# Optimization experiments

Hardware: AMD Instinct MI355X
Metric: run time of the kernel (lower is better)

The kernel has to match this reference:

```python
import jax, jax.numpy as jnp
import numpy as np

N_FEATURES = 1024
N_HEADS = 16
DEPTH = N_FEATURES // N_HEADS


def setup_inputs() -> dict:
    key = jax.random.key(0)
    ks = jax.random.split(key, 12)
    B, S, D = 2, 2048, N_FEATURES
    s = 1.0 / np.sqrt(D)
    return {
        "q": jax.random.normal(ks[0], (B, S, D), jnp.float32),
        "k": jax.random.normal(ks[1], (B, S, D), jnp.float32),
        "v": jax.random.normal(ks[2], (B, S, D), jnp.float32),
        "w_q": jax.random.normal(ks[3], (D, D), jnp.float32) * s,
        "b_q": jnp.zeros((D,), jnp.float32),
        "w_k": jax.random.normal(ks[4], (D, D), jnp.float32) * s,
        "b_k": jnp.zeros((D,), jnp.float32),
        "w_v": jax.random.normal(ks[5], (D, D), jnp.float32) * s,
        "b_v": jnp.zeros((D,), jnp.float32),
        "w_o": jax.random.normal(ks[6], (D, D), jnp.float32) * s,
        "b_o": jnp.zeros((D,), jnp.float32),
    }


def _split_heads(x):
    # [B, S, D] -> [B, H, S, depth]
    B, S, _ = x.shape
    return x.reshape(B, S, N_HEADS, DEPTH).transpose(0, 2, 1, 3)


def reference(q, k, v, w_q, b_q, w_k, b_k, w_v, b_v, w_o, b_o):
    B, S, D = q.shape
    qh = _split_heads(q @ w_q + b_q)  # [B,H,S,d]
    kh = _split_heads(k @ w_k + b_k)
    vh = _split_heads(v @ w_v + b_v)
    scale = 1.0 / jnp.sqrt(jnp.asarray(DEPTH, jnp.float32))
    logits = jnp.einsum("bhqd,bhkd->bhqk", qh, kh) * scale  # [B,H,S,S]
    attn_weights = jax.nn.softmax(logits, axis=-1)
    attn = jnp.einsum("bhqk,bhkd->bhqd", attn_weights, vh)
    concat = attn.transpose(0, 2, 1, 3).reshape(B, S, D)
    output = concat @ w_o + b_o
    return output, attn_weights
```

## Files before the change

kernel.cpp:

```cpp
#include <hip/hip_runtime.h>

typedef __attribute__((ext_vector_type(8))) short short8;
typedef __attribute__((ext_vector_type(4))) float f32x4;

#define MFMA_BF16(A,B,C) __builtin_amdgcn_mfma_f32_16x16x32_bf16((A),(B),(C),0,0,0)

#define SCALE_LOG2E 0.18033688011112043f

__device__ __forceinline__ unsigned short f2bu(float f) {
  unsigned int u = __float_as_uint(f);
  u += 0x7fffu + ((u >> 16) & 1u);
  return (unsigned short)(u >> 16);
}
__device__ __forceinline__ float bu2f(unsigned short u) {
  return __uint_as_float(((unsigned int)u) << 16);
}
__device__ __forceinline__ void gload16(const void* g, void* l) {
  __builtin_amdgcn_global_load_lds(
      (const __attribute__((address_space(1))) void*)g,
      (__attribute__((address_space(3))) void*)l, 16, 0, 0);
}
#define WAITV0 asm volatile("s_waitcnt vmcnt(0)" ::: "memory")
#define WAITV4 asm volatile("s_waitcnt vmcnt(4)" ::: "memory")
__device__ __forceinline__ void barrier_fence() {
  __builtin_amdgcn_s_barrier();
  __builtin_amdgcn_sched_barrier(0);
}

struct PrepArgs {
  const float* src[7];
  unsigned short* dst[7];
};
__global__ __launch_bounds__(256) void prep_kernel(PrepArgs a) {
  __shared__ float t[32][33];
  if (blockIdx.y < 3) {
    const int w = blockIdx.y;
    const int i = blockIdx.x * 256 + threadIdx.x;
    const float4 v = reinterpret_cast<const float4*>(a.src[w])[i];
    ushort4 o;
    o.x = f2bu(v.x); o.y = f2bu(v.y); o.z = f2bu(v.z); o.w = f2bu(v.w);
    reinterpret_cast<ushort4*>(a.dst[w])[i] = o;
  } else {
    const int m = blockIdx.x >> 10;
    const float* w = a.src[3 + m];
    unsigned short* wt = a.dst[3 + m];
    const int bx = ((blockIdx.x >> 5) & 31) * 32;
    const int by = (blockIdx.x & 31) * 32;
    const int tx = threadIdx.x & 31, ty = threadIdx.x >> 5;
    for (int j = 0; j < 4; ++j)
      t[ty + 8 * j][tx] = w[(size_t)(bx + ty + 8 * j) * 1024 + by + tx];
    __syncthreads();
    for (int j = 0; j < 4; ++j)
      wt[(size_t)(by + ty + 8 * j) * 1024 + bx + tx] = f2bu(t[tx][ty + 8 * j]);
  }
}

template <int OUT_MODE>
__device__ __forceinline__ void gemm_core(
    unsigned short* g_lds,
    const unsigned short* __restrict__ A, const unsigned short* __restrict__ Wt,
    const float* __restrict__ bias, void* __restrict__ Cout, int M0, int N0) {
  const int tid = threadIdx.x, lane = tid & 63, wid = tid >> 6;
  const int lr = lane & 15, lg = lane >> 4;
  const int wr = wid >> 2, wc = wid & 3;
  const int srow = lane >> 3, slot = lane & 7;
  f32x4 acc[4][2];
#pragma unroll
  for (int m = 0; m < 4; ++m)
#pragma unroll
    for (int n = 0; n < 2; ++n) acc[m][n] = (f32x4){0.f, 0.f, 0.f, 0.f};

#define G_STAGE(buf, kk)                                                             \
  {                                                                                  \
    _Pragma("unroll") for (int i_ = 0; i_ < 2; ++i_) {                               \
      int idx_ = wid * 2 + i_;                                                       \
      int row_ = idx_ * 8 + srow;                                                    \
      int gs_ = slot ^ (row_ & 7);                                                   \
      gload16(&A[(size_t)(M0 + row_) * 1024 + (kk) + gs_ * 8],                       \
              (char*)g_lds + (buf) * 32768 + idx_ * 1024);                           \
      gload16(&Wt[(size_t)(N0 + row_) * 1024 + (kk) + gs_ * 8],                      \
              (char*)g_lds + (buf) * 32768 + 16384 + idx_ * 1024);                   \
    }                                                                                \
  }

  G_STAGE(0, 0);
  __syncthreads();
  for (int kt = 0; kt < 16; ++kt) {
    const int cur = kt & 1;
    if (kt < 15) G_STAGE(cur ^ 1, (kt + 1) * 64);
    short8 af[4][2], bf[2][2];
#pragma unroll
    for (int m = 0; m < 4; ++m)
#pragma unroll
      for (int kh = 0; kh < 2; ++kh) {
        int row = wr * 64 + m * 16 + lr;
        int s = (kh * 4 + lg) ^ (row & 7);
        af[m][kh] = *reinterpret_cast<const short8*>((const char*)g_lds + cur * 32768 + row * 128 + s * 16);
      }
#pragma unroll
    for (int n = 0; n < 2; ++n)
#pragma unroll
      for (int kh = 0; kh < 2; ++kh) {
        int row = wc * 32 + n * 16 + lr;
        int s = (kh * 4 + lg) ^ (row & 7);
        bf[n][kh] = *reinterpret_cast<const short8*>((const char*)g_lds + cur * 32768 + 16384 + row * 128 + s * 16);
      }
#pragma unroll
    for (int kh = 0; kh < 2; ++kh)
#pragma unroll
      for (int m = 0; m < 4; ++m)
#pragma unroll
        for (int n = 0; n < 2; ++n)
          acc[m][n] = MFMA_BF16(af[m][kh], bf[n][kh], acc[m][n]);
    __syncthreads();
  }

  if (OUT_MODE != 2) {
#pragma unroll
    for (int m = 0; m < 4; ++m)
#pragma unroll
      for (int n = 0; n < 2; ++n)
#pragma unroll
        for (int r = 0; r < 4; ++r) {
          int grow = M0 + wr * 64 + m * 16 + lg * 4 + r;
          int gcol = N0 + wc * 32 + n * 16 + lr;
          float vv = acc[m][n][r] + bias[gcol];
          if (OUT_MODE == 1)
            reinterpret_cast<float*>(Cout)[(size_t)grow * 1024 + gcol] = vv;
          else
            reinterpret_cast<unsigned short*>(Cout)[(size_t)grow * 1024 + gcol] = f2bu(vv);
        }
  } else {
    unsigned short* t = g_lds;
#pragma unroll
    for (int m = 0; m < 4; ++m)
#pragma unroll
      for (int n = 0; n < 2; ++n) {
        int ch = wc * 32 + n * 16 + lr;
        int s4 = wr * 64 + m * 16 + lg * 4;
        int sb = (s4 * 2) ^ ((ch & 7) << 4);
        ushort4 pk;
        pk.x = f2bu(acc[m][n][0] + bias[N0 + ch]);
        pk.y = f2bu(acc[m][n][1] + bias[N0 + ch]);
        pk.z = f2bu(acc[m][n][2] + bias[N0 + ch]);
        pk.w = f2bu(acc[m][n][3] + bias[N0 + ch]);
        *reinterpret_cast<ushort4*>((char*)t + ch * 256 + sb) = pk;
      }
    __syncthreads();
    unsigned short* Vt = (unsigned short*)Cout;
    const int ch = tid >> 2, sc = tid & 3;
    const int bb = M0 >> 11;
    unsigned short* dst = Vt + (size_t)(bb * 1024 + N0 + ch) * 2048 + (M0 & 2047) + sc * 8;
#pragma unroll
    for (int i = 0; i < 4; ++i) {
      int sb = (sc * 16 + i * 64) ^ ((ch & 7) << 4);
      short8 v = *reinterpret_cast<const short8*>((const char*)t + ch * 256 + sb);
      *reinterpret_cast<short8*>(dst + i * 32) = v;
    }
  }
#undef G_STAGE
}

struct Gemm3Args {
  const unsigned short* A[3]; const unsigned short* Wt[3];
  const float* bias[3]; void* C[3];
};
__global__ __launch_bounds__(512) void gemm3_kernel(Gemm3Args a) {
  __shared__ unsigned short g_lds[2 * 16384];
  const int z = blockIdx.z;
  if (z == 2)
    gemm_core<2>(g_lds, a.A[2], a.Wt[2], a.bias[2], a.C[2], blockIdx.x * 128, blockIdx.y * 128);
  else
    gemm_core<0>(g_lds, a.A[z], a.Wt[z], a.bias[z], a.C[z], blockIdx.x * 128, blockIdx.y * 128);
}

__global__ __launch_bounds__(512) void gemm_out_kernel(
    const unsigned short* __restrict__ A, const unsigned short* __restrict__ Wt,
    const float* __restrict__ bias, float* __restrict__ C) {
  __shared__ unsigned short g_lds[2 * 16384];
  gemm_core<1>(g_lds, A, Wt, bias, C, blockIdx.x * 128, blockIdx.y * 128);
}

__global__ __launch_bounds__(512) void attn_den_kernel(
    const unsigned short* __restrict__ Qp, const unsigned short* __restrict__ Kp,
    float* __restrict__ invl_g) {
  __shared__ unsigned short k_lds[2][8192];
  const int bid = ((blockIdx.x & 7) << 6) | (blockIdx.x >> 3);
  const int qt = bid & 15, h = (bid >> 4) & 15, b = bid >> 8;
  const int tid = threadIdx.x, lane = tid & 63, wid = tid >> 6;
  const int lr = lane & 15, lg = lane >> 4;
  const int q0 = qt * 128;
  const int srow = lane >> 3, slot = lane & 7;

  short8 aq[2];
#pragma unroll
  for (int kh = 0; kh < 2; ++kh)
    aq[kh] = *reinterpret_cast<const short8*>(
        &Qp[(size_t)(b * 2048 + q0 + wid * 16 + lr) * 1024 + h * 64 + kh * 32 + lg * 8]);

  const size_t kbase = (size_t)b * 2048 * 1024 + (size_t)(h * 64);

#define KD_STAGE(buf, kk)                                                         \
  {                                                                               \
    _Pragma("unroll") for (int i_ = 0; i_ < 2; ++i_) {                            \
      int idx_ = wid * 2 + i_;                                                    \
      int row_ = idx_ * 8 + srow;                                                 \
      int gs_ = slot ^ (row_ & 7);                                                \
      gload16(&Kp[kbase + (size_t)((kk) + row_) * 1024 + gs_ * 8],                \
              (char*)&k_lds[buf][0] + idx_ * 1024);                               \
    }                                                                             \
  }

  float lsum[4] = {0.f, 0.f, 0.f, 0.f};

  KD_STAGE(0, 0);
  WAITV0;
  barrier_fence();
  for (int kt = 0; kt < 16; ++kt) {
    const int cur = kt & 1;
    if (kt < 15) KD_STAGE(cur ^ 1, (kt + 1) * 128);
    f32x4 lacc[8];
#pragma unroll
    for (int nt = 0; nt < 8; ++nt) lacc[nt] = (f32x4){0.f, 0.f, 0.f, 0.f};
#pragma unroll
    for (int kh = 0; kh < 2; ++kh)
#pragma unroll
      for (int nt = 0; nt < 8; ++nt) {
        int row = nt * 16 + lr;
        int s = (kh * 4 + lg) ^ (row & 7);
        short8 kb = *reinterpret_cast<const short8*>((const char*)&k_lds[cur][0] + row * 128 + s * 16);
        lacc[nt] = MFMA_BF16(aq[kh], kb, lacc[nt]);
      }
#pragma unroll
    for (int nt = 0; nt < 8; ++nt)
#pragma unroll
      for (int r = 0; r < 4; ++r)
        lsum[r] += exp2f(lacc[nt][r] * SCALE_LOG2E);
    WAITV0;
    barrier_fence();
  }
#pragma unroll
  for (int r = 0; r < 4; ++r) {
    float s = lsum[r];
    s += __shfl_xor(s, 1); s += __shfl_xor(s, 2);
    s += __shfl_xor(s, 4); s += __shfl_xor(s, 8);
    if (lr == 0) invl_g[bid * 128 + wid * 16 + lg * 4 + r] = 1.f / s;
  }
#undef KD_STAGE
}

__global__ __launch_bounds__(512) void attn_pv_kernel(
    const unsigned short* __restrict__ Qp, const unsigned short* __restrict__ Kp,
    const unsigned short* __restrict__ Vt, const float* __restrict__ invl_g,
    float* __restrict__ attnw, unsigned short* __restrict__ attnc) {
  __shared__ unsigned short k_lds[2][4096];
  __shared__ unsigned short vt_lds[2][4096];
  __shared__ unsigned short w_lds[8][16][68];
  const int bid = ((blockIdx.x & 7) << 6) | (blockIdx.x >> 3);
  const int qt = bid & 15, h = (bid >> 4) & 15, b = bid >> 8;
  const int tid = threadIdx.x, lane = tid & 63, wid = tid >> 6;
  const int lr = lane & 15, lg = lane >> 4;
  const int q0 = qt * 128;
  const int srow = lane >> 3, slot = lane & 7;

  short8 aq[2];
#pragma unroll
  for (int kh = 0; kh < 2; ++kh)
    aq[kh] = *reinterpret_cast<const short8*>(
        &Qp[(size_t)(b * 2048 + q0 + wid * 16 + lr) * 1024 + h * 64 + kh * 32 + lg * 8]);

  const f32x4 invl = *reinterpret_cast<const f32x4*>(&invl_g[bid * 128 + wid * 16 + lg * 4]);
  float inv_j[4];
#pragma unroll
  for (int j = 0; j < 4; ++j) inv_j[j] = invl_g[bid * 128 + wid * 16 + 4 * j + lg];

  const size_t kbase = (size_t)b * 2048 * 1024 + (size_t)(h * 64);
  const size_t vtbase = (size_t)(b * 1024 + h * 64) * 2048;

#define K_STAGE(buf, kk)                                                          \
  {                                                                               \
    int row_ = wid * 8 + srow;                                                    \
    int gs_ = slot ^ (row_ & 7);                                                  \
    gload16(&Kp[kbase + (size_t)((kk) + row_) * 1024 + gs_ * 8],                  \
            (char*)&k_lds[buf][0] + wid * 1024);                                  \
  }
#define V_STAGE(buf, kk)                                                          \
  {                                                                               \
    int row_ = wid * 8 + srow;                                                    \
    int gs_ = slot ^ (row_ & 7);                                                  \
    gload16(&Vt[vtbase + (size_t)row_ * 2048 + (kk) + gs_ * 8],                   \
            (char*)&vt_lds[buf][0] + wid * 1024);                                 \
  }

  f32x4 oacc[4];
#pragma unroll
  for (int nt = 0; nt < 4; ++nt) oacc[nt] = (f32x4){0.f, 0.f, 0.f, 0.f};

  const size_t wrowb = (size_t)((b * 16 + h) * 2048) + q0 + wid * 16;

  K_STAGE(0, 0);
  V_STAGE(0, 0);
  WAITV0;
  barrier_fence();
  for (int kt = 0; kt < 32; ++kt) {
    const int cur = kt & 1;
    const int k0 = kt * 64;
    if (kt < 31) { K_STAGE(cur ^ 1, k0 + 64); V_STAGE(cur ^ 1, k0 + 64); }
    f32x4 lacc[4];
#pragma unroll
    for (int nt = 0; nt < 4; ++nt) lacc[nt] = (f32x4){0.f, 0.f, 0.f, 0.f};
#pragma unroll
    for (int kh = 0; kh < 2; ++kh)
#pragma unroll
      for (int nt = 0; nt < 4; ++nt) {
        int row = nt * 16 + lr;
        int s = (kh * 4 + lg) ^ (row & 7);
        short8 kb = *reinterpret_cast<const short8*>((const char*)&k_lds[cur][0] + row * 128 + s * 16);
        lacc[nt] = MFMA_BF16(aq[kh], kb, lacc[nt]);
      }
#pragma unroll
    for (int nt = 0; nt < 4; ++nt)
#pragma unroll
      for (int r = 0; r < 4; ++r)
        w_lds[wid][lg * 4 + r][nt * 16 + lr] = f2bu(exp2f(lacc[nt][r] * SCALE_LOG2E));
#pragma unroll
    for (int ks = 0; ks < 2; ++ks) {
      short8 wa = *reinterpret_cast<const short8*>(&w_lds[wid][lr][ks * 32 + lg * 8]);
#pragma unroll
      for (int nt = 0; nt < 4; ++nt) {
        int row = nt * 16 + lr;
        int s = (ks * 4 + lg) ^ (row & 7);
        short8 vb = *reinterpret_cast<const short8*>((const char*)&vt_lds[cur][0] + row * 128 + s * 16);
        oacc[nt] = MFMA_BF16(wa, vb, oacc[nt]);
      }
    }
#pragma unroll
    for (int j = 0; j < 4; ++j) {
      int rowl = 4 * j + lg;
      ushort4 wv = *reinterpret_cast<const ushort4*>(&w_lds[wid][rowl][lr * 4]);
      f32x4 o;
      o[0] = bu2f(wv.x) * inv_j[j];
      o[1] = bu2f(wv.y) * inv_j[j];
      o[2] = bu2f(wv.z) * inv_j[j];
      o[3] = bu2f(wv.w) * inv_j[j];
      __builtin_nontemporal_store(o, reinterpret_cast<f32x4*>(&attnw[(wrowb + rowl) * 2048 + k0 + lr * 4]));
    }
    WAITV4;
    barrier_fence();
  }
#pragma unroll
  for (int nt = 0; nt < 4; ++nt)
#pragma unroll
    for (int r = 0; r < 4; ++r) {
      int srow2 = q0 + wid * 16 + lg * 4 + r;
      attnc[(size_t)(b * 2048 + srow2) * 1024 + h * 64 + nt * 16 + lr] =
          f2bu(oacc[nt][r] * invl[r]);
    }
#undef K_STAGE
#undef V_STAGE
}

extern "C" void kernel_launch(void* const* d_in, const int* in_sizes, int n_in,
                              void* d_out, int out_size, void* d_ws, size_t ws_size,
                              hipStream_t stream) {
  const float* q = (const float*)d_in[0];
  const float* k = (const float*)d_in[1];
  const float* v = (const float*)d_in[2];
  const float* w_q = (const float*)d_in[3];
  const float* b_q = (const float*)d_in[4];
  const float* w_k = (const float*)d_in[5];
  const float* b_k = (const float*)d_in[6];
  const float* w_v = (const float*)d_in[7];
  const float* b_v = (const float*)d_in[8];
  const float* w_o = (const float*)d_in[9];
  const float* b_o = (const float*)d_in[10];

  unsigned short* ws = (unsigned short*)d_ws;
  unsigned short* Qp    = ws;
  unsigned short* Kp    = ws + 4194304;
  unsigned short* Vt    = ws + 8388608;
  unsigned short* attnc = ws + 12582912;
  unsigned short* wqt = ws + 16777216;
  unsigned short* wkt = wqt + 1048576;
  unsigned short* wvt = wkt + 1048576;
  unsigned short* wot = wvt + 1048576;
  float* invl_g = (float*)wqt;

  float* outO = (float*)d_out;
  float* attnw = outO + 4194304;

  unsigned short* qb = (unsigned short*)attnw;
  unsigned short* kb = qb + 4194304;
  unsigned short* vb = kb + 4194304;

  PrepArgs pa;
  pa.src[0] = q; pa.src[1] = k; pa.src[2] = v;
  pa.src[3] = w_q; pa.src[4] = w_k; pa.src[5] = w_v; pa.src[6] = w_o;
  pa.dst[0] = qb; pa.dst[1] = kb; pa.dst[2] = vb;
  pa.dst[3] = wqt; pa.dst[4] = wkt; pa.dst[5] = wvt; pa.dst[6] = wot;
  prep_kernel<<<dim3(4096, 4), 256, 0, stream>>>(pa);

  Gemm3Args ga;
  ga.A[0] = qb; ga.A[1] = kb; ga.A[2] = vb;
  ga.Wt[0] = wqt; ga.Wt[1] = wkt; ga.Wt[2] = wvt;
  ga.bias[0] = b_q; ga.bias[1] = b_k; ga.bias[2] = b_v;
  ga.C[0] = Qp; ga.C[1] = Kp; ga.C[2] = Vt;
  gemm3_kernel<<<dim3(32, 8, 3), 512, 0, stream>>>(ga);

  attn_den_kernel<<<512, 512, 0, stream>>>(Qp, Kp, invl_g);
  attn_pv_kernel<<<512, 512, 0, stream>>>(Qp, Kp, Vt, invl_g, attnw, attnc);

  gemm_out_kernel<<<dim3(32, 8), 512, 0, stream>>>(attnc, wot, b_o, outO);
}
```

Baseline: 229.3 us.

## Fuse attention denominator and PV passes into one kernel with shared LDS

Merges the separate softmax-denominator kernel and the weights/PV kernel into one kernel. The first phase computes row sums of exp(logits), reduces them and keeps the reciprocal in LDS instead of a global buffer, and the second phase reuses the same LDS region for K/V staging. MFMA operands are swapped so each lane holds a whole row segment, which gives a simpler cross-lane reduction and allows packed bf16 conversion (v_cvt_pk_bf16_f32) with vectorised LDS writes of the weights. This removes a kernel launch and a global round trip for the denominators, but each block now runs both passes back to back and uses more LDS.

```diff
diff --git a/kernel.cpp b/kernel.cpp
--- a/kernel.cpp
+++ b/kernel.cpp
@@ -14,6 +14,11 @@
 }
 __device__ __forceinline__ float bu2f(unsigned short u) {
   return __uint_as_float(((unsigned int)u) << 16);
+}
+__device__ __forceinline__ unsigned int cvtpk(float a, float b) {
+  unsigned int r;
+  asm("v_cvt_pk_bf16_f32 %0, %1, %2" : "=v"(r) : "v"(a), "v"(b));
+  return r;
 }
 __device__ __forceinline__ void gload16(const void* g, void* l) {
   __builtin_amdgcn_global_load_lds(
@@ -181,16 +186,20 @@
   gemm_core<1>(g_lds, A, Wt, bias, C, blockIdx.x * 128, blockIdx.y * 128);
 }
 
-__global__ __launch_bounds__(512) void attn_den_kernel(
+__global__ __launch_bounds__(512) void attn_kernel(
     const unsigned short* __restrict__ Qp, const unsigned short* __restrict__ Kp,
-    float* __restrict__ invl_g) {
-  __shared__ unsigned short k_lds[2][8192];
+    const unsigned short* __restrict__ Vt, float* __restrict__ attnw,
+    unsigned short* __restrict__ attnc) {
+  __shared__ unsigned short kv_lds[32768 / 2];
+  __shared__ unsigned short w_lds[8][16][72];
+  __shared__ float linv_lds[128];
   const int bid = ((blockIdx.x & 7) << 6) | (blockIdx.x >> 3);
   const int qt = bid & 15, h = (bid >> 4) & 15, b = bid >> 8;
   const int tid = threadIdx.x, lane = tid & 63, wid = tid >> 6;
   const int lr = lane & 15, lg = lane >> 4;
   const int q0 = qt * 128;
   const int srow = lane >> 3, slot = lane & 7;
+  char* kv = (char*)kv_lds;
 
   short8 aq[2];
 #pragma unroll
@@ -199,6 +208,7 @@
         &Qp[(size_t)(b * 2048 + q0 + wid * 16 + lr) * 1024 + h * 64 + kh * 32 + lg * 8]);
 
   const size_t kbase = (size_t)b * 2048 * 1024 + (size_t)(h * 64);
+  const size_t vtbase = (size_t)(b * 1024 + h * 64) * 2048;
 
 #define KD_STAGE(buf, kk)                                                         \
   {                                                                               \
@@ -207,12 +217,11 @@
       int row_ = idx_ * 8 + srow;                                                 \
       int gs_ = slot ^ (row_ & 7);                                                \
       gload16(&Kp[kbase + (size_t)((kk) + row_) * 1024 + gs_ * 8],                \
-              (char*)&k_lds[buf][0] + idx_ * 1024);                               \
+              kv + (buf) * 16384 + idx_ * 1024);                                  \
     }                                                                             \
   }
 
-  float lsum[4] = {0.f, 0.f, 0.f, 0.f};
-
+  float lsum = 0.f;
   KD_STAGE(0, 0);
   WAITV0;
   barrier_fence();
@@ -228,68 +237,41 @@
       for (int nt = 0; nt < 8; ++nt) {
         int row = nt * 16 + lr;
         int s = (kh * 4 + lg) ^ (row & 7);
-        short8 kb = *reinterpret_cast<const short8*>((const char*)&k_lds[cur][0] + row * 128 + s * 16);
-        lacc[nt] = MFMA_BF16(aq[kh], kb, lacc[nt]);
+        short8 kb = *reinterpret_cast<const short8*>(kv + cur * 16384 + row * 128 + s * 16);
+        lacc[nt] = MFMA_BF16(kb, aq[kh], lacc[nt]);
       }
 #pragma unroll
     for (int nt = 0; nt < 8; ++nt)
 #pragma unroll
       for (int r = 0; r < 4; ++r)
-        lsum[r] += exp2f(lacc[nt][r] * SCALE_LOG2E);
+        lsum += exp2f(lacc[nt][r] * SCALE_LOG2E);
     WAITV0;
     barrier_fence();
   }
-#pragma unroll
-  for (int r = 0; r < 4; ++r) {
-    float s = lsum[r];
-    s += __shfl_xor(s, 1); s += __shfl_xor(s, 2);
-    s += __shfl_xor(s, 4); s += __shfl_xor(s, 8);
-    if (lr == 0) invl_g[bid * 128 + wid * 16 + lg * 4 + r] = 1.f / s;
-  }
-#undef KD_STAGE
-}
-
-__global__ __launch_bounds__(512) void attn_pv_kernel(
-    const unsigned short* __restrict__ Qp, const unsigned short* __restrict__ Kp,
-    const unsigned short* __restrict__ Vt, const float* __restrict__ invl_g,
-    float* __restrict__ attnw, unsigned short* __restrict__ attnc) {
-  __shared__ unsigned short k_lds[2][4096];
-  __shared__ unsigned short vt_lds[2][4096];
-  __shared__ unsigned short w_lds[8][16][68];
-  const int bid = ((blockIdx.x & 7) << 6) | (blockIdx.x >> 3);
-  const int qt = bid & 15, h = (bid >> 4) & 15, b = bid >> 8;
-  const int tid = threadIdx.x, lane = tid & 63, wid = tid >> 6;
-  const int lr = lane & 15, lg = lane >> 4;
-  const int q0 = qt * 128;
-  const int srow = lane >> 3, slot = lane & 7;
-
-  short8 aq[2];
-#pragma unroll
-  for (int kh = 0; kh < 2; ++kh)
-    aq[kh] = *reinterpret_cast<const short8*>(
-        &Qp[(size_t)(b * 2048 + q0 + wid * 16 + lr) * 1024 + h * 64 + kh * 32 + lg * 8]);
-
-  const f32x4 invl = *reinterpret_cast<const f32x4*>(&invl_g[bid * 128 + wid * 16 + lg * 4]);
+  {
+    float s = lsum;
+    s += __shfl_xor(s, 16);
+    s += __shfl_xor(s, 32);
+    if (lg == 0) linv_lds[wid * 16 + lr] = 1.f / s;
+  }
+  const f32x4 invl = *reinterpret_cast<const f32x4*>(&linv_lds[wid * 16 + lg * 4]);
   float inv_j[4];
 #pragma unroll
-  for (int j = 0; j < 4; ++j) inv_j[j] = invl_g[bid * 128 + wid * 16 + 4 * j + lg];
-
-  const size_t kbase = (size_t)b * 2048 * 1024 + (size_t)(h * 64);
-  const size_t vtbase = (size_t)(b * 1024 + h * 64) * 2048;
+  for (int j = 0; j < 4; ++j) inv_j[j] = linv_lds[wid * 16 + 4 * j + lg];
 
 #define K_STAGE(buf, kk)                                                          \
   {                                                                               \
     int row_ = wid * 8 + srow;                                                    \
     int gs_ = slot ^ (row_ & 7);                                                  \
     gload16(&Kp[kbase + (size_t)((kk) + row_) * 1024 + gs_ * 8],                  \
-            (char*)&k_lds[buf][0] + wid * 1024);                                  \
+            kv + (buf) * 8192 + wid * 1024);                                      \
   }
 #define V_STAGE(buf, kk)                                                          \
   {                                                                               \
     int row_ = wid * 8 + srow;                                                    \
     int gs_ = slot ^ (row_ & 7);                                                  \
     gload16(&Vt[vtbase + (size_t)row_ * 2048 + (kk) + gs_ * 8],                   \
-            (char*)&vt_lds[buf][0] + wid * 1024);                                 \
+            kv + 16384 + (buf) * 8192 + wid * 1024);                              \
   }
 
   f32x4 oacc[4];
@@ -315,14 +297,20 @@
       for (int nt = 0; nt < 4; ++nt) {
         int row = nt * 16 + lr;
         int s = (kh * 4 + lg) ^ (row & 7);
-        short8 kb = *reinterpret_cast<const short8*>((const char*)&k_lds[cur][0] + row * 128 + s * 16);
-        lacc[nt] = MFMA_BF16(aq[kh], kb, lacc[nt]);
-      }
-#pragma unroll
-    for (int nt = 0; nt < 4; ++nt)
-#pragma unroll
-      for (int r = 0; r < 4; ++r)
-        w_lds[wid][lg * 4 + r][nt * 16 + lr] = f2bu(exp2f(lacc[nt][r] * SCALE_LOG2E));
+        short8 kb = *reinterpret_cast<const short8*>(kv + cur * 8192 + row * 128 + s * 16);
+        lacc[nt] = MFMA_BF16(kb, aq[kh], lacc[nt]);
+      }
+#pragma unroll
+    for (int nt = 0; nt < 4; ++nt) {
+      float e0 = exp2f(lacc[nt][0] * SCALE_LOG2E);
+      float e1 = exp2f(lacc[nt][1] * SCALE_LOG2E);
+      float e2 = exp2f(lacc[nt][2] * SCALE_LOG2E);
+      float e3 = exp2f(lacc[nt][3] * SCALE_LOG2E);
+      uint2 pk;
+      pk.x = cvtpk(e0, e1);
+      pk.y = cvtpk(e2, e3);
+      *reinterpret_cast<uint2*>(&w_lds[wid][lr][nt * 16 + lg * 4]) = pk;
+    }
 #pragma unroll
     for (int ks = 0; ks < 2; ++ks) {
       short8 wa = *reinterpret_cast<const short8*>(&w_lds[wid][lr][ks * 32 + lg * 8]);
@@ -330,7 +318,7 @@
       for (int nt = 0; nt < 4; ++nt) {
         int row = nt * 16 + lr;
         int s = (ks * 4 + lg) ^ (row & 7);
-        short8 vb = *reinterpret_cast<const short8*>((const char*)&vt_lds[cur][0] + row * 128 + s * 16);
+        short8 vb = *reinterpret_cast<const short8*>(kv + 16384 + cur * 8192 + row * 128 + s * 16);
         oacc[nt] = MFMA_BF16(wa, vb, oacc[nt]);
       }
     }
@@ -356,6 +344,7 @@
       attnc[(size_t)(b * 2048 + srow2) * 1024 + h * 64 + nt * 16 + lr] =
           f2bu(oacc[nt][r] * invl[r]);
     }
+#undef KD_STAGE
 #undef K_STAGE
 #undef V_STAGE
 }
@@ -384,7 +373,6 @@
   unsigned short* wkt = wqt + 1048576;
   unsigned short* wvt = wkt + 1048576;
   unsigned short* wot = wvt + 1048576;
-  float* invl_g = (float*)wqt;
 
   float* outO = (float*)d_out;
   float* attnw = outO + 4194304;
@@ -407,8 +395,7 @@
   ga.C[0] = Qp; ga.C[1] = Kp; ga.C[2] = Vt;
   gemm3_kernel<<<dim3(32, 8, 3), 512, 0, stream>>>(ga);
 
-  attn_den_kernel<<<512, 512, 0, stream>>>(Qp, Kp, invl_g);
-  attn_pv_kernel<<<512, 512, 0, stream>>>(Qp, Kp, Vt, invl_g, attnw, attnc);
+  attn_kernel<<<512, 512, 0, stream>>>(Qp, Kp, Vt, attnw, attnc);
 
   gemm_out_kernel<<<dim3(32, 8), 512, 0, stream>>>(attnc, wot, b_o, outO);
 }
```

New measurement: 211.1 us. -7.9%, faster.
